# Kernel optimization log

Measured on AMD Instinct MI355X. Metric: run time of the kernel, lower is better.

The kernel has to match this reference:

```python
import jax, jax.numpy as jnp
import numpy as np

N = 8192
IN_F = 128
OUT_F = 64
ALPHA = 0.2  # LeakyReLU negative slope
NEG_INF = -1.0e9


def setup_inputs() -> dict:
    key = jax.random.key(0)
    k_x, k_adj, k_W, k_a = jax.random.split(key, 4)
    x = jax.random.normal(k_x, (N, IN_F), dtype=jnp.float32)
    adj = (jax.random.uniform(k_adj, (N, N)) < 0.02).astype(jnp.float32)
    adj = jnp.maximum(adj, jnp.eye(N, dtype=jnp.float32))
    W = jax.random.normal(k_W, (IN_F, OUT_F), dtype=jnp.float32) * (1.414 / np.sqrt(IN_F))
    a = jax.random.normal(k_a, (2 * OUT_F, 1), dtype=jnp.float32) * 0.1
    return {"x": x, "adj": adj, "W": W, "a": a}


def reference(x, adj, W, a):
    # h: [N, out_f]
    h = x @ W
    # GAT scores: e_ij = leakyrelu(a1.h_i + a2.h_j), dense [N, N]
    h_i = h @ a[:OUT_F]            # [N, 1]
    h_j = h @ a[OUT_F:]            # [N, 1]
    e = h_i + h_j.T                # [N, N]
    e = jax.nn.leaky_relu(e, negative_slope=ALPHA)
    # mask non-edges (adj <= 0) with -1e9, then row softmax
    attn_logits = jnp.where(adj > 0, e, NEG_INF)
    attn = jax.nn.softmax(attn_logits, axis=-1)
    # weighted aggregate + ELU (dropout is identity at p=0 / eval)
    out = jax.nn.elu(attn @ h)
    return out
```

## Files before the change

### kernel.cpp

```cpp
#include <hip/hip_runtime.h>
#include <hip/hip_bf16.h>

#define N_NODES 8192
#define IN_F 128
#define OUT_F 64
#define ALPHA 0.2f
#define CAP 128
#define WT_STRIDE 132

__global__ __launch_bounds__(256, 4) void gat_h(
    const float* __restrict__ x, const float* __restrict__ W,
    const float* __restrict__ a, float* __restrict__ h,
    float* __restrict__ hi, float* __restrict__ hj) {
  __shared__ float sWt[OUT_F][WT_STRIDE];
  int tid = threadIdx.x;
  for (int i = tid; i < IN_F * OUT_F; i += 256) {
    int k = i >> 6, f = i & 63;
    sWt[f][k] = W[i];
  }
  __syncthreads();

  int lane = tid & 63;
  int wid = tid >> 6;
  float a1 = a[lane], a2 = a[OUT_F + lane];
  int row0 = blockIdx.x * 8;

  for (int rr = 0; rr < 2; ++rr) {
    int row = row0 + rr * 4 + wid;
    const float4* xr = (const float4*)(x + (size_t)row * IN_F);
    float acc = 0.f;
#pragma unroll
    for (int k4 = 0; k4 < IN_F / 4; ++k4) {
      float4 xv = xr[k4];
      float4 wv = *(const float4*)&sWt[lane][k4 * 4];
      acc = fmaf(xv.x, wv.x, acc);
      acc = fmaf(xv.y, wv.y, acc);
      acc = fmaf(xv.z, wv.z, acc);
      acc = fmaf(xv.w, wv.w, acc);
    }
    h[(size_t)row * 64 + lane] = acc;
    float vi = acc * a1, vj = acc * a2;
#pragma unroll
    for (int o = 32; o >= 1; o >>= 1) {
      vi += __shfl_xor(vi, o);
      vj += __shfl_xor(vj, o);
    }
    if (lane == 0) { hi[row] = vi; hj[row] = vj; }
  }
}

__global__ __launch_bounds__(256, 4) void gat_row(
    const float* __restrict__ adj, const float* __restrict__ h,
    const float* __restrict__ hi, const float* __restrict__ hj,
    float* __restrict__ out) {
  __shared__ int s_idx[4][CAP];
  __shared__ float s_w[4][CAP];
  __shared__ float s_psum[4];
  __shared__ float s_part[4][64];

  int tid = threadIdx.x;
  int lane = tid & 63;
  int wid = tid >> 6;
  int row = blockIdx.x;

  const float4* aq = (const float4*)(adj + (size_t)row * N_NODES) + wid * 512;
  unsigned int mk = 0;
#pragma unroll
  for (int it = 0; it < 8; ++it) {
    float4 vv = aq[lane + it * 64];
    mk |= (unsigned int)(vv.x > 0.f) << (it * 4 + 0);
    mk |= (unsigned int)(vv.y > 0.f) << (it * 4 + 1);
    mk |= (unsigned int)(vv.z > 0.f) << (it * 4 + 2);
    mk |= (unsigned int)(vv.w > 0.f) << (it * 4 + 3);
  }
  int c = __popc(mk);

  int incl = c;
#pragma unroll
  for (int o = 1; o < 64; o <<= 1) {
    int t = __shfl_up(incl, o);
    if (lane >= o) incl += t;
  }
  int off = incl - c;
  int cnt = __shfl(incl, 63);
  if (cnt > CAP) cnt = CAP;

  int* widx = s_idx[wid];
  float* ww = s_w[wid];
  float hii = hi[row];
  float psum = 0.f;
  while (mk) {
    int b = __ffs(mk) - 1;
    mk &= mk - 1;
    int j = (wid << 11) + (lane << 2) + ((b >> 2) << 8) + (b & 3);
    float l = hii + hj[j];
    l = (l > 0.f) ? l : ALPHA * l;
    float w = __expf(l);
    if (off < CAP) { widx[off] = j; ww[off] = w; }
    ++off;
    psum += w;
  }
  int cnp = (cnt + 7) & ~7;
  if (lane < cnp - cnt) { ww[cnt + lane] = 0.f; widx[cnt + lane] = 0; }
#pragma unroll
  for (int o = 32; o >= 1; o >>= 1) psum += __shfl_xor(psum, o);
  if (lane == 0) s_psum[wid] = psum;
  __syncthreads();
  float inv = 1.f / (s_psum[0] + s_psum[1] + s_psum[2] + s_psum[3]);

  float acc0 = 0.f, acc1 = 0.f, acc2 = 0.f, acc3 = 0.f;
  float acc4 = 0.f, acc5 = 0.f, acc6 = 0.f, acc7 = 0.f;
  for (int e = 0; e < cnp; e += 8) {
    int4 ia = *(const int4*)&widx[e];
    int4 ib = *(const int4*)&widx[e + 4];
    float4 wa = *(const float4*)&ww[e];
    float4 wb = *(const float4*)&ww[e + 4];
    acc0 = fmaf(wa.x, h[(size_t)ia.x * 64 + lane], acc0);
    acc1 = fmaf(wa.y, h[(size_t)ia.y * 64 + lane], acc1);
    acc2 = fmaf(wa.z, h[(size_t)ia.z * 64 + lane], acc2);
    acc3 = fmaf(wa.w, h[(size_t)ia.w * 64 + lane], acc3);
    acc4 = fmaf(wb.x, h[(size_t)ib.x * 64 + lane], acc4);
    acc5 = fmaf(wb.y, h[(size_t)ib.y * 64 + lane], acc5);
    acc6 = fmaf(wb.z, h[(size_t)ib.z * 64 + lane], acc6);
    acc7 = fmaf(wb.w, h[(size_t)ib.w * 64 + lane], acc7);
  }
  s_part[wid][lane] =
      ((acc0 + acc1) + (acc2 + acc3)) + ((acc4 + acc5) + (acc6 + acc7));
  __syncthreads();
  if (tid < 64) {
    float vv = s_part[0][tid] + s_part[1][tid] + s_part[2][tid] + s_part[3][tid];
    vv *= inv;
    vv = (vv > 0.f) ? vv : expm1f(vv);
    out[(size_t)row * 64 + tid] = vv;
  }
}

extern "C" void kernel_launch(void* const* d_in, const int* in_sizes, int n_in,
                              void* d_out, int out_size, void* d_ws, size_t ws_size,
                              hipStream_t stream) {
  const float* x   = (const float*)d_in[0];
  const float* adj = (const float*)d_in[1];
  const float* W   = (const float*)d_in[2];
  const float* a   = (const float*)d_in[3];
  float* out = (float*)d_out;

  float* h  = (float*)d_ws;
  float* hi = h + (size_t)N_NODES * OUT_F;
  float* hj = hi + N_NODES;

  gat_h<<<N_NODES / 8, 256, 0, stream>>>(x, W, a, h, hi, hj);
  gat_row<<<N_NODES, 256, 0, stream>>>(adj, h, hi, hj, out);
}
```

Before: 98.79 us.

## Use block-wide interleaved adjacency load and shared edge list across warps

Adjacency rows are now read with block-wide interleaved float4 loads: all eight loads are issued up front, and an empty asm barrier keeps them in flight together. Per-warp edge counts are combined through shared memory into one block-wide compacted list with a larger capacity. The four warps then split the gather-FMA loop by interleaving 8-edge chunks, so aggregation work is balanced across warps instead of tied to each warp's column slice. This adds an extra __syncthreads and more shared memory, and it raises the per-row cap on stored edges.

```diff
diff --git a/kernel.cpp b/kernel.cpp
--- a/kernel.cpp
+++ b/kernel.cpp
@@ -5,8 +5,10 @@
 #define IN_F 128
 #define OUT_F 64
 #define ALPHA 0.2f
-#define CAP 128
+#define CAPB 1024
 #define WT_STRIDE 132
+
+typedef __attribute__((ext_vector_type(4))) float f32x4;
 
 __global__ __launch_bounds__(256, 4) void gat_h(
     const float* __restrict__ x, const float* __restrict__ W,
@@ -53,8 +55,9 @@
     const float* __restrict__ adj, const float* __restrict__ h,
     const float* __restrict__ hi, const float* __restrict__ hj,
     float* __restrict__ out) {
-  __shared__ int s_idx[4][CAP];
-  __shared__ float s_w[4][CAP];
+  __shared__ int s_idx[CAPB + 32];
+  __shared__ float s_w[CAPB + 32];
+  __shared__ int s_tot[4];
   __shared__ float s_psum[4];
   __shared__ float s_part[4][64];
 
@@ -63,16 +66,27 @@
   int wid = tid >> 6;
   int row = blockIdx.x;
 
-  const float4* aq = (const float4*)(adj + (size_t)row * N_NODES) + wid * 512;
+  const f32x4* arow = (const f32x4*)(adj + (size_t)row * N_NODES);
+  f32x4 v0 = arow[tid];
+  f32x4 v1 = arow[tid + 256];
+  f32x4 v2 = arow[tid + 512];
+  f32x4 v3 = arow[tid + 768];
+  f32x4 v4 = arow[tid + 1024];
+  f32x4 v5 = arow[tid + 1280];
+  f32x4 v6 = arow[tid + 1536];
+  f32x4 v7 = arow[tid + 1792];
+  asm volatile("" : "+v"(v0), "+v"(v1), "+v"(v2), "+v"(v3),
+                    "+v"(v4), "+v"(v5), "+v"(v6), "+v"(v7));
+
   unsigned int mk = 0;
-#pragma unroll
-  for (int it = 0; it < 8; ++it) {
-    float4 vv = aq[lane + it * 64];
-    mk |= (unsigned int)(vv.x > 0.f) << (it * 4 + 0);
-    mk |= (unsigned int)(vv.y > 0.f) << (it * 4 + 1);
-    mk |= (unsigned int)(vv.z > 0.f) << (it * 4 + 2);
-    mk |= (unsigned int)(vv.w > 0.f) << (it * 4 + 3);
-  }
+#define MASK4(v, it)                                   \
+  mk |= (unsigned int)(v.x > 0.f) << (it * 4 + 0);     \
+  mk |= (unsigned int)(v.y > 0.f) << (it * 4 + 1);     \
+  mk |= (unsigned int)(v.z > 0.f) << (it * 4 + 2);     \
+  mk |= (unsigned int)(v.w > 0.f) << (it * 4 + 3);
+  MASK4(v0, 0) MASK4(v1, 1) MASK4(v2, 2) MASK4(v3, 3)
+  MASK4(v4, 4) MASK4(v5, 5) MASK4(v6, 6) MASK4(v7, 7)
+#undef MASK4
   int c = __popc(mk);
 
   int incl = c;
@@ -81,27 +95,29 @@
     int t = __shfl_up(incl, o);
     if (lane >= o) incl += t;
   }
-  int off = incl - c;
-  int cnt = __shfl(incl, 63);
-  if (cnt > CAP) cnt = CAP;
+  if (lane == 63) s_tot[wid] = incl;
+  __syncthreads();
+  int t0 = s_tot[0], t1 = s_tot[1], t2 = s_tot[2], t3 = s_tot[3];
+  int base = (wid > 0 ? t0 : 0) + (wid > 1 ? t1 : 0) + (wid > 2 ? t2 : 0);
+  int off = base + incl - c;
+  int cnt = t0 + t1 + t2 + t3;
+  if (cnt > CAPB) cnt = CAPB;
+  int cnp = (cnt + 31) & ~31;
 
-  int* widx = s_idx[wid];
-  float* ww = s_w[wid];
   float hii = hi[row];
   float psum = 0.f;
   while (mk) {
     int b = __ffs(mk) - 1;
     mk &= mk - 1;
-    int j = (wid << 11) + (lane << 2) + ((b >> 2) << 8) + (b & 3);
+    int j = (tid << 2) + ((b >> 2) << 10) + (b & 3);
     float l = hii + hj[j];
     l = (l > 0.f) ? l : ALPHA * l;
     float w = __expf(l);
-    if (off < CAP) { widx[off] = j; ww[off] = w; }
+    if (off < CAPB) { s_idx[off] = j; s_w[off] = w; }
     ++off;
     psum += w;
   }
-  int cnp = (cnt + 7) & ~7;
-  if (lane < cnp - cnt) { ww[cnt + lane] = 0.f; widx[cnt + lane] = 0; }
+  for (int e = cnt + tid; e < cnp; e += 256) { s_w[e] = 0.f; s_idx[e] = 0; }
 #pragma unroll
   for (int o = 32; o >= 1; o >>= 1) psum += __shfl_xor(psum, o);
   if (lane == 0) s_psum[wid] = psum;
@@ -110,11 +126,11 @@
 
   float acc0 = 0.f, acc1 = 0.f, acc2 = 0.f, acc3 = 0.f;
   float acc4 = 0.f, acc5 = 0.f, acc6 = 0.f, acc7 = 0.f;
-  for (int e = 0; e < cnp; e += 8) {
-    int4 ia = *(const int4*)&widx[e];
-    int4 ib = *(const int4*)&widx[e + 4];
-    float4 wa = *(const float4*)&ww[e];
-    float4 wb = *(const float4*)&ww[e + 4];
+  for (int e = wid * 8; e < cnp; e += 32) {
+    int4 ia = *(const int4*)&s_idx[e];
+    int4 ib = *(const int4*)&s_idx[e + 4];
+    float4 wa = *(const float4*)&s_w[e];
+    float4 wb = *(const float4*)&s_w[e + 4];
     acc0 = fmaf(wa.x, h[(size_t)ia.x * 64 + lane], acc0);
     acc1 = fmaf(wa.y, h[(size_t)ia.y * 64 + lane], acc1);
     acc2 = fmaf(wa.z, h[(size_t)ia.z * 64 + lane], acc2);
```

Result: no change. 100.5 us (+1.7%).
